# Optimization experiments

Measured on AMD Instinct MI355X. Metric: run time of the kernel, lower is better.

Reference implementation:

```python
import jax, jax.numpy as jnp
import numpy as np

EPS = 1e-8
K = 3  # num_neighbors

def setup_inputs() -> dict:
    key = jax.random.key(0)
    k1, k2, k3, k4 = jax.random.split(key, 4)
    n, B, m, C = 16384, 8, 2048, 128
    return {
        "unknown": jax.random.normal(k1, (n, 3), dtype=jnp.float32),
        "known": jax.random.normal(k2, (B, m, 3), dtype=jnp.float32),
        "batch_inds": jax.random.randint(k3, (n,), 0, B),
        "known_feats": jax.random.normal(k4, (B, C, m), dtype=jnp.float32),
    }

def reference(unknown, known, batch_inds, known_feats):
    # unknown: (n,3); known: (B,m,3); batch_inds: (n,); known_feats: (B,C,m)
    kg = known[batch_inds]                                   # (n,m,3) gather per-query scene
    d2 = jnp.sum((unknown[:, None, :] - kg) ** 2, axis=-1)   # (n,m) squared L2
    neg_d2, idx = jax.lax.top_k(-d2, K)                      # 3 nearest (sorted ascending dist)
    dist = jnp.sqrt(jnp.maximum(-neg_d2, 0.0))               # (n,K)
    dist_recip = 1.0 / (dist + EPS)
    weight = dist_recip / jnp.sum(dist_recip, axis=-1, keepdims=True)  # (n,K)
    # gather neighbor features: (n,K,C)
    feats = known_feats[batch_inds[:, None], :, idx]
    out = jnp.einsum('nkc,nk->nc', feats, weight)            # (n,C)
    return out[:, :, None]                                   # (n,C,1)
```

## Files before the change

### kernel.cpp

```cpp
#include <hip/hip_runtime.h>

#define NPTS 16384
#define NB   8
#define NM   2048
#define NC   128
#define EPSF 1e-8f

#define TQ   16
#define QPB  16
#define GX   160

#define MERGE_KEY(e) do {                               \
    const bool _b2 = (e) < K2;                          \
    const bool _b1 = (e) < K1;                          \
    const bool _b0 = (e) < K0;                          \
    K2 = _b1 ? K1 : (_b2 ? (e) : K2);                   \
    K1 = _b0 ? K0 : (_b1 ? (e) : K1);                   \
    K0 = _b0 ? (e) : K0;                                \
} while (0)

__global__ __launch_bounds__(256, 5) void fused(const float* __restrict__ unknown,
                                                const float* __restrict__ known,
                                                const int*   __restrict__ binds,
                                                const float* __restrict__ feats,
                                                float* __restrict__ out) {
    __shared__ float2 kxy[NM];
    __shared__ float  kz[NM];
    __shared__ int qlist[QPB];
    __shared__ int wsum[4];

    const int tid  = threadIdx.x;
    const int b    = blockIdx.y;
    const int x    = blockIdx.x;
    const int lane = tid & 63;
    const int wave = tid >> 6;

    const int4* b4 = (const int4*)binds;
    int myCnt = 0;
#pragma unroll
    for (int r = 0; r < 16; ++r) {
        const int4 v = b4[tid * 16 + r];
        myCnt += (v.x == b) + (v.y == b) + (v.z == b) + (v.w == b);
    }
    int inc = myCnt;
#pragma unroll
    for (int off = 1; off <= 32; off <<= 1) {
        const int n = __shfl_up(inc, off);
        if (lane >= off) inc += n;
    }
    if (lane == 63) wsum[wave] = inc;
    __syncthreads();
    int wbase = 0;
    for (int w = 0; w < wave; ++w) wbase += wsum[w];
    const int exPre = wbase + inc - myCnt;
    const int segN  = wsum[0] + wsum[1] + wsum[2] + wsum[3];

    if (x * QPB >= segN) return;

    {
        const float* kb = known + (size_t)b * NM * 3;
        for (int j = tid; j < NM; j += 256) {
            float2 xy; xy.x = kb[j * 3 + 0]; xy.y = kb[j * 3 + 1];
            kxy[j] = xy;
            kz[j]  = kb[j * 3 + 2];
        }
    }

    const int qi = tid >> 4;
    const int t  = tid & 15;

    for (int w0 = x * QPB; w0 < segN; w0 += GX * QPB) {
        __syncthreads();
        if (exPre < w0 + QPB && exPre + myCnt > w0) {
            int rank = exPre;
#pragma unroll
            for (int r = 0; r < 16; ++r) {
                const int4 v = b4[tid * 16 + r];
                const int base = tid * 64 + r * 4;
                if (v.x == b) { if (rank >= w0 && rank < w0 + QPB) qlist[rank - w0] = base + 0; ++rank; }
                if (v.y == b) { if (rank >= w0 && rank < w0 + QPB) qlist[rank - w0] = base + 1; ++rank; }
                if (v.z == b) { if (rank >= w0 && rank < w0 + QPB) qlist[rank - w0] = base + 2; ++rank; }
                if (v.w == b) { if (rank >= w0 && rank < w0 + QPB) qlist[rank - w0] = base + 3; ++rank; }
            }
        }
        __syncthreads();

        const int valid = (segN - w0 < QPB) ? (segN - w0) : QPB;
        const int kq    = (qi < valid) ? qi : 0;
        const int p     = qlist[kq];
        const float ux = unknown[p * 3 + 0];
        const float uy = unknown[p * 3 + 1];
        const float uz = unknown[p * 3 + 2];

        unsigned long long K0 = ~0ull, K1 = ~0ull, K2 = ~0ull;

#pragma unroll 8
        for (int i = 0; i < NM / TQ; ++i) {
            const int j = (i << 4) | t;
            const float2 kp = kxy[j];
            const float  kzz = kz[j];
            const float dx = __fsub_rn(ux, kp.x);
            const float dy = __fsub_rn(uy, kp.y);
            const float dz = __fsub_rn(uz, kzz);
            const float d  = __fadd_rn(__fadd_rn(__fmul_rn(dx, dx), __fmul_rn(dy, dy)),
                                       __fmul_rn(dz, dz));
            const unsigned long long key =
                ((unsigned long long)__float_as_uint(d) << 32) | (unsigned)j;
            MERGE_KEY(key);
        }

#pragma unroll
        for (int off = 8; off >= 1; off >>= 1) {
            const unsigned long long e0 = __shfl_down(K0, off);
            const unsigned long long e1 = __shfl_down(K1, off);
            const unsigned long long e2 = __shfl_down(K2, off);
            MERGE_KEY(e0);
            MERGE_KEY(e1);
            MERGE_KEY(e2);
        }
        const int src = lane & ~15;
        K0 = __shfl(K0, src); K1 = __shfl(K1, src); K2 = __shfl(K2, src);

        const float d0 = __uint_as_float((unsigned)(K0 >> 32));
        const float d1 = __uint_as_float((unsigned)(K1 >> 32));
        const float d2 = __uint_as_float((unsigned)(K2 >> 32));
        const int   i0 = (int)(unsigned)K0;
        const int   i1 = (int)(unsigned)K1;
        const int   i2 = (int)(unsigned)K2;

        const float t0 = 1.0f / (sqrtf(d0) + EPSF);
        const float t1 = 1.0f / (sqrtf(d1) + EPSF);
        const float t2 = 1.0f / (sqrtf(d2) + EPSF);
        const float s  = t0 + t1 + t2;
        const float w0w = t0 / s, w1w = t1 / s, w2w = t2 / s;

        const float* fb = feats + (size_t)b * NC * NM;
#pragma unroll
        for (int k = 0; k < 8; ++k) {
            const int c = t + (k << 4);
            const float* fc = fb + (size_t)c * NM;
            const float f0 = fc[i0];
            const float f1 = fc[i1];
            const float f2 = fc[i2];
            out[(size_t)p * NC + c] = w0w * f0 + w1w * f1 + w2w * f2;
        }
    }
}

extern "C" void kernel_launch(void* const* d_in, const int* in_sizes, int n_in,
                              void* d_out, int out_size, void* d_ws, size_t ws_size,
                              hipStream_t stream) {
    const float* unknown = (const float*)d_in[0];
    const float* known   = (const float*)d_in[1];
    const int*   binds   = (const int*)d_in[2];
    const float* feats   = (const float*)d_in[3];
    float*       out     = (float*)d_out;

    fused<<<dim3(GX, NB), 256, 0, stream>>>(unknown, known, binds, feats, out);
}
```

Before: 112.6 us.

## Transpose features to point-major layout for vectorized neighbor gathers

Adds a pre-pass kernel that transposes known_feats from (B,C,m) to (B,m,C) in the workspace, so each neighbor's channel vector can be read contiguously with float4 loads instead of strided scalar gathers. It also packs known points into float4 shared memory and lowers the occupancy hint from 5 to 4. The transpose adds a full extra read and write of the 8 MB feature tensor plus a kernel launch on every call. The original gather path remains as a fallback when the workspace is too small.

```diff
diff --git a/kernel.cpp b/kernel.cpp
--- a/kernel.cpp
+++ b/kernel.cpp
@@ -9,6 +9,8 @@
 #define TQ   16
 #define QPB  16
 #define GX   160
+
+#define FEATST_BYTES ((size_t)NB * NM * NC * sizeof(float))
 
 #define MERGE_KEY(e) do {                               \
     const bool _b2 = (e) < K2;                          \
@@ -19,13 +21,31 @@
     K0 = _b0 ? (e) : K0;                                \
 } while (0)
 
-__global__ __launch_bounds__(256, 5) void fused(const float* __restrict__ unknown,
+__global__ __launch_bounds__(256) void transpose_feats(const float* __restrict__ in,
+                                                       float* __restrict__ out) {
+    __shared__ float tile[32][33];
+    const int b  = blockIdx.z;
+    const int j0 = blockIdx.x * 32;
+    const int c0 = blockIdx.y * 32;
+    const int tx = threadIdx.x;
+    const int ty = threadIdx.y;
+#pragma unroll
+    for (int i = ty; i < 32; i += 8)
+        tile[i][tx] = in[(size_t)b * NC * NM + (size_t)(c0 + i) * NM + (j0 + tx)];
+    __syncthreads();
+#pragma unroll
+    for (int i = ty; i < 32; i += 8)
+        out[(size_t)b * NM * NC + (size_t)(j0 + i) * NC + (c0 + tx)] = tile[tx][i];
+}
+
+__global__ __launch_bounds__(256, 4) void fused(const float* __restrict__ unknown,
                                                 const float* __restrict__ known,
                                                 const int*   __restrict__ binds,
                                                 const float* __restrict__ feats,
-                                                float* __restrict__ out) {
-    __shared__ float2 kxy[NM];
-    __shared__ float  kz[NM];
+                                                const float* __restrict__ featsT,
+                                                float* __restrict__ out,
+                                                int useT) {
+    __shared__ float4 kpt[NM];
     __shared__ int qlist[QPB];
     __shared__ int wsum[4];
 
@@ -60,9 +80,12 @@
     {
         const float* kb = known + (size_t)b * NM * 3;
         for (int j = tid; j < NM; j += 256) {
-            float2 xy; xy.x = kb[j * 3 + 0]; xy.y = kb[j * 3 + 1];
-            kxy[j] = xy;
-            kz[j]  = kb[j * 3 + 2];
+            float4 kp;
+            kp.x = kb[j * 3 + 0];
+            kp.y = kb[j * 3 + 1];
+            kp.z = kb[j * 3 + 2];
+            kp.w = 0.0f;
+            kpt[j] = kp;
         }
     }
 
@@ -97,11 +120,10 @@
 #pragma unroll 8
         for (int i = 0; i < NM / TQ; ++i) {
             const int j = (i << 4) | t;
-            const float2 kp = kxy[j];
-            const float  kzz = kz[j];
+            const float4 kp = kpt[j];
             const float dx = __fsub_rn(ux, kp.x);
             const float dy = __fsub_rn(uy, kp.y);
-            const float dz = __fsub_rn(uz, kzz);
+            const float dz = __fsub_rn(uz, kp.z);
             const float d  = __fadd_rn(__fadd_rn(__fmul_rn(dx, dx), __fmul_rn(dy, dy)),
                                        __fmul_rn(dz, dz));
             const unsigned long long key =
@@ -134,15 +156,31 @@
         const float s  = t0 + t1 + t2;
         const float w0w = t0 / s, w1w = t1 / s, w2w = t2 / s;
 
-        const float* fb = feats + (size_t)b * NC * NM;
-#pragma unroll
-        for (int k = 0; k < 8; ++k) {
-            const int c = t + (k << 4);
-            const float* fc = fb + (size_t)c * NM;
-            const float f0 = fc[i0];
-            const float f1 = fc[i1];
-            const float f2 = fc[i2];
-            out[(size_t)p * NC + c] = w0w * f0 + w1w * f1 + w2w * f2;
+        if (useT) {
+            const float4* ftb = (const float4*)(featsT + (size_t)b * NM * NC);
+            const float4* f0 = ftb + (size_t)i0 * (NC / 4);
+            const float4* f1 = ftb + (size_t)i1 * (NC / 4);
+            const float4* f2 = ftb + (size_t)i2 * (NC / 4);
+            float4* o4 = (float4*)(out + (size_t)p * NC);
+#pragma unroll
+            for (int k = 0; k < 2; ++k) {
+                const int c4 = t + k * 16;
+                const float4 a = f0[c4], bb = f1[c4], cc = f2[c4];
+                float4 r;
+                r.x = w0w * a.x + w1w * bb.x + w2w * cc.x;
+                r.y = w0w * a.y + w1w * bb.y + w2w * cc.y;
+                r.z = w0w * a.z + w1w * bb.z + w2w * cc.z;
+                r.w = w0w * a.w + w1w * bb.w + w2w * cc.w;
+                o4[c4] = r;
+            }
+        } else {
+            const float* fb = feats + (size_t)b * NC * NM;
+#pragma unroll
+            for (int k = 0; k < 8; ++k) {
+                const int c = t + (k << 4);
+                const float* fc = fb + (size_t)c * NM;
+                out[(size_t)p * NC + c] = w0w * fc[i0] + w1w * fc[i1] + w2w * fc[i2];
+            }
         }
     }
 }
@@ -156,5 +194,13 @@
     const float* feats   = (const float*)d_in[3];
     float*       out     = (float*)d_out;
 
-    fused<<<dim3(GX, NB), 256, 0, stream>>>(unknown, known, binds, feats, out);
+    const int useT = (ws_size >= FEATST_BYTES) ? 1 : 0;
+    float* featsT = (float*)d_ws;
+
+    if (useT) {
+        dim3 tb(32, 8, 1);
+        dim3 tg(NM / 32, NC / 32, NB);
+        transpose_feats<<<tg, tb, 0, stream>>>(feats, featsT);
+    }
+    fused<<<dim3(GX, NB), 256, 0, stream>>>(unknown, known, binds, feats, featsT, out, useT);
 }
```

Result: slower. 120.8 us (+7.2%).

## Process two queries per thread with register-prefetched known points

Applied to the files above, without the earlier changes.

Each thread now scans known points for two queries at once, with 32 threads per query pair instead of 16 threads per query, so every LDS load of a known point serves two distance computations. The next point is prefetched into registers before the current one is computed. The shuffle reduction grows to 32 lanes, and the feature gather/write loop handles both queries with a 32-wide channel stride. Register pressure rises, so the launch bound is lowered from 5 to 4 blocks per CU, which may reduce occupancy.

```diff
diff --git a/kernel.cpp b/kernel.cpp
--- a/kernel.cpp
+++ b/kernel.cpp
@@ -6,11 +6,12 @@
 #define NC   128
 #define EPSF 1e-8f
 
-#define TQ   16
+#define TQ   32
+#define QPT  2
 #define QPB  16
 #define GX   160
 
-#define MERGE_KEY(e) do {                               \
+#define MERGE_KEY(K0, K1, K2, e) do {                   \
     const bool _b2 = (e) < K2;                          \
     const bool _b1 = (e) < K1;                          \
     const bool _b0 = (e) < K0;                          \
@@ -19,7 +20,7 @@
     K0 = _b0 ? (e) : K0;                                \
 } while (0)
 
-__global__ __launch_bounds__(256, 5) void fused(const float* __restrict__ unknown,
+__global__ __launch_bounds__(256, 4) void fused(const float* __restrict__ unknown,
                                                 const float* __restrict__ known,
                                                 const int*   __restrict__ binds,
                                                 const float* __restrict__ feats,
@@ -66,8 +67,8 @@
         }
     }
 
-    const int qi = tid >> 4;
-    const int t  = tid & 15;
+    const int g = tid >> 5;
+    const int t = tid & 31;
 
     for (int w0 = x * QPB; w0 < segN; w0 += GX * QPB) {
         __syncthreads();
@@ -86,63 +87,94 @@
         __syncthreads();
 
         const int valid = (segN - w0 < QPB) ? (segN - w0) : QPB;
-        const int kq    = (qi < valid) ? qi : 0;
-        const int p     = qlist[kq];
-        const float ux = unknown[p * 3 + 0];
-        const float uy = unknown[p * 3 + 1];
-        const float uz = unknown[p * 3 + 2];
+        const int q0i   = (2 * g + 0 < valid) ? (2 * g + 0) : 0;
+        const int q1i   = (2 * g + 1 < valid) ? (2 * g + 1) : 0;
+        const int pA    = qlist[q0i];
+        const int pB    = qlist[q1i];
+        const float uxA = unknown[pA * 3 + 0], uyA = unknown[pA * 3 + 1], uzA = unknown[pA * 3 + 2];
+        const float uxB = unknown[pB * 3 + 0], uyB = unknown[pB * 3 + 1], uzB = unknown[pB * 3 + 2];
 
-        unsigned long long K0 = ~0ull, K1 = ~0ull, K2 = ~0ull;
+        unsigned long long A0 = ~0ull, A1 = ~0ull, A2 = ~0ull;
+        unsigned long long B0 = ~0ull, B1 = ~0ull, B2 = ~0ull;
 
-#pragma unroll 8
+        float2 xy = kxy[t];
+        float  zz = kz[t];
+#pragma unroll 4
         for (int i = 0; i < NM / TQ; ++i) {
-            const int j = (i << 4) | t;
-            const float2 kp = kxy[j];
-            const float  kzz = kz[j];
-            const float dx = __fsub_rn(ux, kp.x);
-            const float dy = __fsub_rn(uy, kp.y);
-            const float dz = __fsub_rn(uz, kzz);
-            const float d  = __fadd_rn(__fadd_rn(__fmul_rn(dx, dx), __fmul_rn(dy, dy)),
-                                       __fmul_rn(dz, dz));
-            const unsigned long long key =
-                ((unsigned long long)__float_as_uint(d) << 32) | (unsigned)j;
-            MERGE_KEY(key);
+            const int j = (i << 5) | t;
+            const float2 cxy = xy;
+            const float  cz  = zz;
+            if (i + 1 < NM / TQ) {
+                xy = kxy[j + TQ];
+                zz = kz[j + TQ];
+            }
+            const float dxA = __fsub_rn(uxA, cxy.x);
+            const float dyA = __fsub_rn(uyA, cxy.y);
+            const float dzA = __fsub_rn(uzA, cz);
+            const float dA  = __fadd_rn(__fadd_rn(__fmul_rn(dxA, dxA), __fmul_rn(dyA, dyA)),
+                                        __fmul_rn(dzA, dzA));
+            const float dxB = __fsub_rn(uxB, cxy.x);
+            const float dyB = __fsub_rn(uyB, cxy.y);
+            const float dzB = __fsub_rn(uzB, cz);
+            const float dB  = __fadd_rn(__fadd_rn(__fmul_rn(dxB, dxB), __fmul_rn(dyB, dyB)),
+                                        __fmul_rn(dzB, dzB));
+            const unsigned long long keyA =
+                ((unsigned long long)__float_as_uint(dA) << 32) | (unsigned)j;
+            const unsigned long long keyB =
+                ((unsigned long long)__float_as_uint(dB) << 32) | (unsigned)j;
+            MERGE_KEY(A0, A1, A2, keyA);
+            MERGE_KEY(B0, B1, B2, keyB);
         }
 
 #pragma unroll
-        for (int off = 8; off >= 1; off >>= 1) {
-            const unsigned long long e0 = __shfl_down(K0, off);
-            const unsigned long long e1 = __shfl_down(K1, off);
-            const unsigned long long e2 = __shfl_down(K2, off);
-            MERGE_KEY(e0);
-            MERGE_KEY(e1);
-            MERGE_KEY(e2);
+        for (int off = 16; off >= 1; off >>= 1) {
+            const unsigned long long a0 = __shfl_down(A0, off);
+            const unsigned long long a1 = __shfl_down(A1, off);
+            const unsigned long long a2 = __shfl_down(A2, off);
+            MERGE_KEY(A0, A1, A2, a0);
+            MERGE_KEY(A0, A1, A2, a1);
+            MERGE_KEY(A0, A1, A2, a2);
+            const unsigned long long c0 = __shfl_down(B0, off);
+            const unsigned long long c1 = __shfl_down(B1, off);
+            const unsigned long long c2 = __shfl_down(B2, off);
+            MERGE_KEY(B0, B1, B2, c0);
+            MERGE_KEY(B0, B1, B2, c1);
+            MERGE_KEY(B0, B1, B2, c2);
         }
-        const int src = lane & ~15;
-        K0 = __shfl(K0, src); K1 = __shfl(K1, src); K2 = __shfl(K2, src);
-
-        const float d0 = __uint_as_float((unsigned)(K0 >> 32));
-        const float d1 = __uint_as_float((unsigned)(K1 >> 32));
-        const float d2 = __uint_as_float((unsigned)(K2 >> 32));
-        const int   i0 = (int)(unsigned)K0;
-        const int   i1 = (int)(unsigned)K1;
-        const int   i2 = (int)(unsigned)K2;
-
-        const float t0 = 1.0f / (sqrtf(d0) + EPSF);
-        const float t1 = 1.0f / (sqrtf(d1) + EPSF);
-        const float t2 = 1.0f / (sqrtf(d2) + EPSF);
-        const float s  = t0 + t1 + t2;
-        const float w0w = t0 / s, w1w = t1 / s, w2w = t2 / s;
+        const int src = lane & ~31;
+        A0 = __shfl(A0, src); A1 = __shfl(A1, src); A2 = __shfl(A2, src);
+        B0 = __shfl(B0, src); B1 = __shfl(B1, src); B2 = __shfl(B2, src);
 
         const float* fb = feats + (size_t)b * NC * NM;
 #pragma unroll
-        for (int k = 0; k < 8; ++k) {
-            const int c = t + (k << 4);
-            const float* fc = fb + (size_t)c * NM;
-            const float f0 = fc[i0];
-            const float f1 = fc[i1];
-            const float f2 = fc[i2];
-            out[(size_t)p * NC + c] = w0w * f0 + w1w * f1 + w2w * f2;
+        for (int q = 0; q < QPT; ++q) {
+            const unsigned long long K0 = q ? B0 : A0;
+            const unsigned long long K1 = q ? B1 : A1;
+            const unsigned long long K2 = q ? B2 : A2;
+            const int p = q ? pB : pA;
+
+            const float d0 = __uint_as_float((unsigned)(K0 >> 32));
+            const float d1 = __uint_as_float((unsigned)(K1 >> 32));
+            const float d2 = __uint_as_float((unsigned)(K2 >> 32));
+            const int   i0 = (int)(unsigned)K0;
+            const int   i1 = (int)(unsigned)K1;
+            const int   i2 = (int)(unsigned)K2;
+
+            const float t0 = 1.0f / (sqrtf(d0) + EPSF);
+            const float t1 = 1.0f / (sqrtf(d1) + EPSF);
+            const float t2 = 1.0f / (sqrtf(d2) + EPSF);
+            const float s  = t0 + t1 + t2;
+            const float w0w = t0 / s, w1w = t1 / s, w2w = t2 / s;
+
+#pragma unroll
+            for (int k = 0; k < 4; ++k) {
+                const int c = t + (k << 5);
+                const float* fc = fb + (size_t)c * NM;
+                const float f0 = fc[i0];
+                const float f1 = fc[i1];
+                const float f2 = fc[i2];
+                out[(size_t)p * NC + c] = w0w * f0 + w1w * f1 + w2w * f2;
+            }
         }
     }
 }
```

After: 128.9 us. 14.5% more time.

## Use 512-thread blocks with 32 lanes per query and float4 LDS points

Applied to the files above, without the earlier changes.

Doubles the block to 512 threads so each of the 16 queries per block is scanned by 32 lanes instead of 16, which halves the per-lane distance/top-3 loop and adds one more shuffle-merge round. Known points are packed into a padded float4 shared array and software-prefetched one iteration ahead, replacing the separate float2/float loads. The batch-index counting is re-split across 512 threads and the grid width is reduced. This trades a longer cross-lane reduction and lower register budget per thread for shorter serial scans and more lanes in flight.

```diff
diff --git a/kernel.cpp b/kernel.cpp
--- a/kernel.cpp
+++ b/kernel.cpp
@@ -6,11 +6,11 @@
 #define NC   128
 #define EPSF 1e-8f
 
-#define TQ   16
+#define TQ   32
 #define QPB  16
-#define GX   160
+#define GX   132
 
-#define MERGE_KEY(e) do {                               \
+#define MERGE_KEY(K0, K1, K2, e) do {                   \
     const bool _b2 = (e) < K2;                          \
     const bool _b1 = (e) < K1;                          \
     const bool _b0 = (e) < K0;                          \
@@ -19,15 +19,14 @@
     K0 = _b0 ? (e) : K0;                                \
 } while (0)
 
-__global__ __launch_bounds__(256, 5) void fused(const float* __restrict__ unknown,
+__global__ __launch_bounds__(512, 8) void fused(const float* __restrict__ unknown,
                                                 const float* __restrict__ known,
                                                 const int*   __restrict__ binds,
                                                 const float* __restrict__ feats,
                                                 float* __restrict__ out) {
-    __shared__ float2 kxy[NM];
-    __shared__ float  kz[NM];
+    __shared__ float4 kpt[NM];
     __shared__ int qlist[QPB];
-    __shared__ int wsum[4];
+    __shared__ int wsum[8];
 
     const int tid  = threadIdx.x;
     const int b    = blockIdx.y;
@@ -38,8 +37,8 @@
     const int4* b4 = (const int4*)binds;
     int myCnt = 0;
 #pragma unroll
-    for (int r = 0; r < 16; ++r) {
-        const int4 v = b4[tid * 16 + r];
+    for (int r = 0; r < 8; ++r) {
+        const int4 v = b4[tid * 8 + r];
         myCnt += (v.x == b) + (v.y == b) + (v.z == b) + (v.w == b);
     }
     int inc = myCnt;
@@ -53,30 +52,35 @@
     int wbase = 0;
     for (int w = 0; w < wave; ++w) wbase += wsum[w];
     const int exPre = wbase + inc - myCnt;
-    const int segN  = wsum[0] + wsum[1] + wsum[2] + wsum[3];
+    int segN = 0;
+#pragma unroll
+    for (int w = 0; w < 8; ++w) segN += wsum[w];
 
     if (x * QPB >= segN) return;
 
     {
         const float* kb = known + (size_t)b * NM * 3;
-        for (int j = tid; j < NM; j += 256) {
-            float2 xy; xy.x = kb[j * 3 + 0]; xy.y = kb[j * 3 + 1];
-            kxy[j] = xy;
-            kz[j]  = kb[j * 3 + 2];
+        for (int j = tid; j < NM; j += 512) {
+            float4 kp;
+            kp.x = kb[j * 3 + 0];
+            kp.y = kb[j * 3 + 1];
+            kp.z = kb[j * 3 + 2];
+            kp.w = 0.0f;
+            kpt[j] = kp;
         }
     }
 
-    const int qi = tid >> 4;
-    const int t  = tid & 15;
+    const int g = tid >> 5;
+    const int t = tid & 31;
 
     for (int w0 = x * QPB; w0 < segN; w0 += GX * QPB) {
         __syncthreads();
         if (exPre < w0 + QPB && exPre + myCnt > w0) {
             int rank = exPre;
 #pragma unroll
-            for (int r = 0; r < 16; ++r) {
-                const int4 v = b4[tid * 16 + r];
-                const int base = tid * 64 + r * 4;
+            for (int r = 0; r < 8; ++r) {
+                const int4 v = b4[tid * 8 + r];
+                const int base = tid * 32 + r * 4;
                 if (v.x == b) { if (rank >= w0 && rank < w0 + QPB) qlist[rank - w0] = base + 0; ++rank; }
                 if (v.y == b) { if (rank >= w0 && rank < w0 + QPB) qlist[rank - w0] = base + 1; ++rank; }
                 if (v.z == b) { if (rank >= w0 && rank < w0 + QPB) qlist[rank - w0] = base + 2; ++rank; }
@@ -86,7 +90,7 @@
         __syncthreads();
 
         const int valid = (segN - w0 < QPB) ? (segN - w0) : QPB;
-        const int kq    = (qi < valid) ? qi : 0;
+        const int kq    = (g < valid) ? g : 0;
         const int p     = qlist[kq];
         const float ux = unknown[p * 3 + 0];
         const float uy = unknown[p * 3 + 1];
@@ -94,31 +98,32 @@
 
         unsigned long long K0 = ~0ull, K1 = ~0ull, K2 = ~0ull;
 
-#pragma unroll 8
+        float4 kp = kpt[t];
+#pragma unroll 4
         for (int i = 0; i < NM / TQ; ++i) {
-            const int j = (i << 4) | t;
-            const float2 kp = kxy[j];
-            const float  kzz = kz[j];
-            const float dx = __fsub_rn(ux, kp.x);
-            const float dy = __fsub_rn(uy, kp.y);
-            const float dz = __fsub_rn(uz, kzz);
+            const int j = (i << 5) | t;
+            const float4 c = kp;
+            if (i + 1 < NM / TQ) kp = kpt[j + TQ];
+            const float dx = __fsub_rn(ux, c.x);
+            const float dy = __fsub_rn(uy, c.y);
+            const float dz = __fsub_rn(uz, c.z);
             const float d  = __fadd_rn(__fadd_rn(__fmul_rn(dx, dx), __fmul_rn(dy, dy)),
                                        __fmul_rn(dz, dz));
             const unsigned long long key =
                 ((unsigned long long)__float_as_uint(d) << 32) | (unsigned)j;
-            MERGE_KEY(key);
+            MERGE_KEY(K0, K1, K2, key);
         }
 
 #pragma unroll
-        for (int off = 8; off >= 1; off >>= 1) {
+        for (int off = 16; off >= 1; off >>= 1) {
             const unsigned long long e0 = __shfl_down(K0, off);
             const unsigned long long e1 = __shfl_down(K1, off);
             const unsigned long long e2 = __shfl_down(K2, off);
-            MERGE_KEY(e0);
-            MERGE_KEY(e1);
-            MERGE_KEY(e2);
+            MERGE_KEY(K0, K1, K2, e0);
+            MERGE_KEY(K0, K1, K2, e1);
+            MERGE_KEY(K0, K1, K2, e2);
         }
-        const int src = lane & ~15;
+        const int src = lane & ~31;
         K0 = __shfl(K0, src); K1 = __shfl(K1, src); K2 = __shfl(K2, src);
 
         const float d0 = __uint_as_float((unsigned)(K0 >> 32));
@@ -136,8 +141,8 @@
 
         const float* fb = feats + (size_t)b * NC * NM;
 #pragma unroll
-        for (int k = 0; k < 8; ++k) {
-            const int c = t + (k << 4);
+        for (int k = 0; k < 4; ++k) {
+            const int c = t + (k << 5);
             const float* fc = fb + (size_t)c * NM;
             const float f0 = fc[i0];
             const float f1 = fc[i1];
@@ -156,5 +161,5 @@
     const float* feats   = (const float*)d_in[3];
     float*       out     = (float*)d_out;
 
-    fused<<<dim3(GX, NB), 256, 0, stream>>>(unknown, known, binds, feats, out);
+    fused<<<dim3(GX, NB), 512, 0, stream>>>(unknown, known, binds, feats, out);
 }
```

Result: slower. 120.0 us (+6.5%).
